# Kernel tuning notes

Hardware: AMD Instinct MI355X
Metric: run time of the kernel (lower is better)

The kernel has to match this reference:

```python
import jax, jax.numpy as jnp
import numpy as np

NEG_SLOPE = 0.2  # PyG GATConv leaky_relu slope
N_NODE = 1000   # nodes per graph (= n_nodes ctor arg = lstm1 input_size)
BATCH = 32      # num_graphs
C = 32          # in_channels == GAT out_channels per head
HEADS = 8
E = 384000      # total edges over the batched graph
H1, H2 = 32, 128
N_PRED = 2
N = N_NODE * BATCH


def _lstm(x_seq, W_ih, W_hh, b_ih, b_hh):
    # x_seq: [T, B, In]; PyTorch gate order i,f,g,o
    B = x_seq.shape[1]
    Hd = W_hh.shape[1]
    h0 = jnp.zeros((B, Hd), x_seq.dtype)

    def step(carry, x_t):
        h, c = carry
        g = x_t @ W_ih.T + h @ W_hh.T + b_ih + b_hh
        i, f, gg, o = jnp.split(g, 4, axis=-1)
        c = jax.nn.sigmoid(f) * c + jax.nn.sigmoid(i) * jnp.tanh(gg)
        h = jax.nn.sigmoid(o) * jnp.tanh(c)
        return (h, c), h

    (_, _), hs = jax.lax.scan(step, (h0, h0), x_seq)
    return hs


def setup_inputs() -> dict:
    key = jax.random.key(0)
    ks = jax.random.split(key, 20)
    inp = {}
    inp["x"] = jax.random.normal(ks[0], (N, C), jnp.float32)
    inp["src"] = jax.random.randint(ks[1], (E,), 0, N)
    inp["dst"] = jax.random.randint(ks[2], (E,), 0, N)
    inp["batch_size"] = BATCH
    # GATConv params (concat=False: mean over heads)
    inp["W_gat"] = jax.random.normal(ks[3], (C, HEADS * C), jnp.float32) * 0.1
    inp["a_src"] = jax.random.normal(ks[4], (HEADS, C), jnp.float32) * 0.1
    inp["a_dst"] = jax.random.normal(ks[5], (HEADS, C), jnp.float32) * 0.1
    inp["b_gat"] = jnp.zeros((C,), jnp.float32)
    # LSTM1: input N_NODE -> hidden 32
    inp["W_ih1"] = jax.random.normal(ks[6], (4 * H1, N_NODE), jnp.float32) * 0.05
    inp["W_hh1"] = jax.random.normal(ks[7], (4 * H1, H1), jnp.float32) * 0.1
    inp["b_ih1"] = jnp.zeros((4 * H1,), jnp.float32)
    inp["b_hh1"] = jnp.zeros((4 * H1,), jnp.float32)
    # LSTM2: input 32 -> hidden 128 (repaired from buggy source)
    inp["W_ih2"] = jax.random.normal(ks[8], (4 * H2, H1), jnp.float32) * 0.1
    inp["W_hh2"] = jax.random.normal(ks[9], (4 * H2, H2), jnp.float32) * 0.08
    inp["b_ih2"] = jnp.zeros((4 * H2,), jnp.float32)
    inp["b_hh2"] = jnp.zeros((4 * H2,), jnp.float32)
    # Linear head: 128 -> n_nodes * n_pred
    inp["W_lin"] = jax.random.normal(ks[10], (N_NODE * N_PRED, H2), jnp.float32) * 0.08
    inp["b_lin"] = jnp.zeros((N_NODE * N_PRED,), jnp.float32)
    return inp


def reference(x, src, dst, batch_size, W_gat, a_src, a_dst, b_gat,
              W_ih1, W_hh1, b_ih1, b_hh1, W_ih2, W_hh2, b_ih2, b_hh2,
              W_lin, b_lin):
    n, c = x.shape
    h = a_src.shape[0]
    # --- GATConv ---
    x_lin = (x @ W_gat).reshape(n, h, c)               # [N, H, C]
    asrc = jnp.einsum('nhc,hc->nh', x_lin, a_src)      # [N, H]
    adst = jnp.einsum('nhc,hc->nh', x_lin, a_dst)
    e = jax.nn.leaky_relu(asrc[src] + adst[dst], NEG_SLOPE)   # [E, H]
    m = jax.ops.segment_max(e, dst, num_segments=n)
    m = jnp.where(jnp.isfinite(m), m, 0.0)             # isolated nodes
    ew = jnp.exp(e - m[dst])
    denom = jax.ops.segment_sum(ew, dst, num_segments=n)
    alpha = ew / jnp.maximum(denom[dst], 1e-16)        # segment softmax
    agg = jax.ops.segment_sum(alpha[:, :, None] * x_lin[src], dst, num_segments=n)
    out = agg.mean(axis=1) + b_gat                     # concat=False -> head mean; [N, C]
    # --- reshape: seq over feature dim, LSTM input = nodes-per-graph ---
    n_node = n // batch_size
    seq = jnp.moveaxis(out.reshape(batch_size, n_node, c), 2, 0)  # [C, B, n_node]
    h1 = _lstm(seq, W_ih1, W_hh1, b_ih1, b_hh1)
    h2 = _lstm(h1, W_ih2, W_hh2, b_ih2, b_hh2)
    last = h2[-1]                                       # [B, 128]
    y = last @ W_lin.T + b_lin                          # [B, n_node*n_pred]
    return y.reshape(batch_size * n_node, -1)           # [B*n_node, n_pred]
```

## Files before the change

### kernel.cpp

```cpp
#include <hip/hip_runtime.h>
#include <hip/hip_fp16.h>
#include <math.h>

#define NEG_SLOPE 0.2f

__device__ __forceinline__ float sigm(float x) { return 1.0f / (1.0f + __expf(-x)); }
__device__ __forceinline__ float tanh_fast(float x) {
    float xc = fminf(fmaxf(x, -15.0f), 15.0f);
    float e2 = __expf(2.0f * xc);
    return (e2 - 1.0f) / (e2 + 1.0f);
}
__device__ __forceinline__ float lrelu(float x) { return (x > 0.0f) ? x : NEG_SLOPE * x; }

typedef _Float16 h2v __attribute__((ext_vector_type(2)));
__device__ __forceinline__ float fdot2h(h2v a, h2v b, float c) {
#if __has_builtin(__builtin_amdgcn_fdot2)
    return __builtin_amdgcn_fdot2(a, b, c, false);
#else
    return (float)a[0] * (float)b[0] + (float)a[1] * (float)b[1] + c;
#endif
}

__device__ __forceinline__ float dot16(const uint4& w, const uint4& h, float acc) {
    const h2v* wp = reinterpret_cast<const h2v*>(&w);
    const h2v* hp = reinterpret_cast<const h2v*>(&h);
    acc = fdot2h(wp[0], hp[0], acc);
    acc = fdot2h(wp[1], hp[1], acc);
    acc = fdot2h(wp[2], hp[2], acc);
    acc = fdot2h(wp[3], hp[3], acc);
    return acc;
}

__global__ void k_zero(int* __restrict__ deg, int N) {
    int i = blockIdx.x * 256 + threadIdx.x;
    if (i < N) deg[i] = 0;
}

__global__ void k_hist(const int* __restrict__ dst, int* __restrict__ deg, int E) {
    int e = blockIdx.x * 256 + threadIdx.x;
    if (e < E) atomicAdd(deg + dst[e], 1);
}

__global__ __launch_bounds__(256) void k_scan1(const int* __restrict__ deg,
                                               int* __restrict__ blksum, int N) {
    __shared__ int s[256];
    int tid = threadIdx.x;
    int i = blockIdx.x * 256 + tid;
    int v = (i < N) ? deg[i] : 0;
    s[tid] = v;
    __syncthreads();
    #pragma unroll
    for (int off = 128; off > 0; off >>= 1) {
        if (tid < off) s[tid] += s[tid + off];
        __syncthreads();
    }
    if (tid == 0) blksum[blockIdx.x] = s[0];
}

__global__ __launch_bounds__(256) void k_scan2(const int* __restrict__ blksum,
                                               int* __restrict__ blkoff, int nb) {
    __shared__ int s[256];
    int tid = threadIdx.x;
    int v = (tid < nb) ? blksum[tid] : 0;
    s[tid] = v;
    __syncthreads();
    for (int off = 1; off < 256; off <<= 1) {
        int t = (tid >= off) ? s[tid - off] : 0;
        __syncthreads();
        s[tid] += t;
        __syncthreads();
    }
    if (tid < nb) blkoff[tid] = s[tid] - v;
}

__global__ __launch_bounds__(256) void k_scan3(const int* __restrict__ deg,
                                               const int* __restrict__ blkoff,
                                               int* __restrict__ rowptr,
                                               int* __restrict__ cursor, int N, int E) {
    __shared__ int s[256];
    int tid = threadIdx.x;
    int i = blockIdx.x * 256 + tid;
    int v = (i < N) ? deg[i] : 0;
    s[tid] = v;
    __syncthreads();
    for (int off = 1; off < 256; off <<= 1) {
        int t = (tid >= off) ? s[tid - off] : 0;
        __syncthreads();
        s[tid] += t;
        __syncthreads();
    }
    int excl = s[tid] - v + blkoff[blockIdx.x];
    if (i < N) { rowptr[i] = excl; cursor[i] = excl; }
    if (i == N - 1) rowptr[N] = E;
}

__global__ void k_scatter(const int* __restrict__ src, const int* __restrict__ dst,
                          int* __restrict__ cursor, int* __restrict__ csr_src, int E) {
    int e = blockIdx.x * 256 + threadIdx.x;
    if (e < E) {
        int pos = atomicAdd(cursor + dst[e], 1);
        csr_src[pos] = src[e];
    }
}

__global__ void k_pre(const float* __restrict__ W_gat, const float* __restrict__ a_src,
                      const float* __restrict__ a_dst, float* __restrict__ wa) {
    int tid = threadIdx.x;
    int k = tid >> 3, h = tid & 7;
    float s1 = 0.0f, s2 = 0.0f;
    for (int c = 0; c < 32; ++c) {
        float wv = W_gat[k * 256 + h * 32 + c];
        s1 += wv * a_src[h * 32 + c];
        s2 += wv * a_dst[h * 32 + c];
    }
    wa[tid] = s1;
    wa[256 + tid] = s2;
}

__global__ __launch_bounds__(256) void k_att(const float* __restrict__ x,
                                             const float* __restrict__ wa,
                                             float* __restrict__ asrc,
                                             float* __restrict__ adst) {
    __shared__ float xs[32 * 33];
    __shared__ float was[256], wad[256];
    int tid = threadIdx.x;
    int n0 = blockIdx.x * 32;
    for (int i = tid; i < 1024; i += 256) {
        int nl = i >> 5, k = i & 31;
        xs[nl * 33 + k] = x[(size_t)(n0 + nl) * 32 + k];
    }
    was[tid] = wa[tid];
    wad[tid] = wa[256 + tid];
    __syncthreads();
    int nl = tid >> 3, h = tid & 7;
    float s1 = 0.0f, s2 = 0.0f;
    #pragma unroll
    for (int k = 0; k < 32; ++k) {
        float xv = xs[nl * 33 + k];
        s1 += xv * was[k * 8 + h];
        s2 += xv * wad[k * 8 + h];
    }
    asrc[(size_t)(n0 + nl) * 8 + h] = s1;
    adst[(size_t)(n0 + nl) * 8 + h] = s2;
}

__global__ __launch_bounds__(256) void k_gat(
    const int* __restrict__ rowptr, const int* __restrict__ csr_src,
    const float* __restrict__ asrc, const float* __restrict__ adst,
    const float* __restrict__ x, float* __restrict__ z, int N) {
    int w = (blockIdx.x * 256 + threadIdx.x) >> 6;
    int lane = threadIdx.x & 63;
    if (w >= N) return;
    int r0 = rowptr[w], r1 = rowptr[w + 1];
    int h = lane >> 3, kq = lane & 7;
    float ad = adst[w * 8 + h];
    float4 acc = make_float4(0.0f, 0.0f, 0.0f, 0.0f);
    float den = 0.0f;
    const float4* x4 = (const float4*)x;
    for (int i = r0; i < r1; i += 8) {
        int rem = r1 - i;
        int s0 = csr_src[i];
        int s1 = (rem > 1) ? csr_src[i + 1] : s0;
        int s2 = (rem > 2) ? csr_src[i + 2] : s0;
        int s3 = (rem > 3) ? csr_src[i + 3] : s0;
        int s4 = (rem > 4) ? csr_src[i + 4] : s0;
        int s5 = (rem > 5) ? csr_src[i + 5] : s0;
        int s6 = (rem > 6) ? csr_src[i + 6] : s0;
        int s7 = (rem > 7) ? csr_src[i + 7] : s0;
        float a0 = asrc[s0 * 8 + h], a1 = asrc[s1 * 8 + h];
        float a2 = asrc[s2 * 8 + h], a3 = asrc[s3 * 8 + h];
        float a4 = asrc[s4 * 8 + h], a5 = asrc[s5 * 8 + h];
        float a6 = asrc[s6 * 8 + h], a7 = asrc[s7 * 8 + h];
        float4 v0 = x4[(size_t)s0 * 8 + kq], v1 = x4[(size_t)s1 * 8 + kq];
        float4 v2 = x4[(size_t)s2 * 8 + kq], v3 = x4[(size_t)s3 * 8 + kq];
        float4 v4 = x4[(size_t)s4 * 8 + kq], v5 = x4[(size_t)s5 * 8 + kq];
        float4 v6 = x4[(size_t)s6 * 8 + kq], v7 = x4[(size_t)s7 * 8 + kq];
        float e0 = __expf(lrelu(a0 + ad));
        float e1 = (rem > 1) ? __expf(lrelu(a1 + ad)) : 0.0f;
        float e2 = (rem > 2) ? __expf(lrelu(a2 + ad)) : 0.0f;
        float e3 = (rem > 3) ? __expf(lrelu(a3 + ad)) : 0.0f;
        float e4 = (rem > 4) ? __expf(lrelu(a4 + ad)) : 0.0f;
        float e5 = (rem > 5) ? __expf(lrelu(a5 + ad)) : 0.0f;
        float e6 = (rem > 6) ? __expf(lrelu(a6 + ad)) : 0.0f;
        float e7 = (rem > 7) ? __expf(lrelu(a7 + ad)) : 0.0f;
        acc.x += e0 * v0.x + e1 * v1.x + e2 * v2.x + e3 * v3.x
               + e4 * v4.x + e5 * v5.x + e6 * v6.x + e7 * v7.x;
        acc.y += e0 * v0.y + e1 * v1.y + e2 * v2.y + e3 * v3.y
               + e4 * v4.y + e5 * v5.y + e6 * v6.y + e7 * v7.y;
        acc.z += e0 * v0.z + e1 * v1.z + e2 * v2.z + e3 * v3.z
               + e4 * v4.z + e5 * v5.z + e6 * v6.z + e7 * v7.z;
        acc.w += e0 * v0.w + e1 * v1.w + e2 * v2.w + e3 * v3.w
               + e4 * v4.w + e5 * v5.w + e6 * v6.w + e7 * v7.w;
        den += ((e0 + e1) + (e2 + e3)) + ((e4 + e5) + (e6 + e7));
    }
    float inv = 1.0f / fmaxf(den, 1e-16f);
    float4 r = make_float4(acc.x * inv, acc.y * inv, acc.z * inv, acc.w * inv);
    ((float4*)z)[(size_t)w * 64 + lane] = r;
}

__global__ __launch_bounds__(256) void k_zw(
    const float* __restrict__ z, const float* __restrict__ W_gat,
    const float* __restrict__ b_gat, float* __restrict__ gatT, int N, int n_node) {
    int gw = (blockIdx.x * 256 + threadIdx.x) >> 6;
    int lane = threadIdx.x & 63;
    int chalf = gw & 1;
    int nset = gw >> 1;
    int c = chalf * 16 + (lane & 15);
    int sl = lane >> 4;
    float wcol[64];
    #pragma unroll
    for (int i = 0; i < 64; ++i) {
        int k = i & 31, hh = sl * 2 + (i >> 5);
        wcol[i] = 0.125f * W_gat[k * 256 + hh * 32 + c];
    }
    float bg = b_gat[c];
    const float4* z4 = (const float4*)z;
    #pragma unroll 2
    for (int it = 0; it < 8; ++it) {
        int n = nset * 8 + it;
        float p = 0.0f;
        #pragma unroll
        for (int k4 = 0; k4 < 16; ++k4) {
            float4 zv = z4[(size_t)n * 64 + sl * 16 + k4];
            p += zv.x * wcol[4 * k4] + zv.y * wcol[4 * k4 + 1]
               + zv.z * wcol[4 * k4 + 2] + zv.w * wcol[4 * k4 + 3];
        }
        p += __shfl_xor(p, 16, 64);
        p += __shfl_xor(p, 32, 64);
        if (lane < 16) {
            int b = n / n_node, kk = n - b * n_node;
            gatT[((size_t)b * 32 + c) * n_node + kk] = p + bg;
        }
    }
}

__global__ __launch_bounds__(256) void k_wt(const float* __restrict__ W,
                                            float* __restrict__ Wt, int n_node) {
    __shared__ float tle[32][33];
    int kt = blockIdx.x & 31;
    int gt = blockIdx.x >> 5;
    int tid = threadIdx.x;
    for (int i = tid; i < 1024; i += 256) {
        int gl = i >> 5, kl = i & 31;
        int g = gt * 32 + gl, k = kt * 32 + kl;
        tle[gl][kl] = (k < n_node) ? W[(size_t)g * n_node + k] : 0.0f;
    }
    __syncthreads();
    for (int i = tid; i < 1024; i += 256) {
        int kl = i >> 5, gl = i & 31;
        int k = kt * 32 + kl, g = gt * 32 + gl;
        if (k < n_node) Wt[(size_t)k * 128 + g] = tle[gl][kl];
    }
}

__global__ __launch_bounds__(256) void k_pack2(
    const float* __restrict__ W_hh2, const float* __restrict__ W_ih2,
    const float* __restrict__ W_hh1,
    uint4* __restrict__ wc2p, uint4* __restrict__ wi2p, uint4* __restrict__ w1p) {
    int i = blockIdx.x * 256 + threadIdx.x;
    __align__(16) _Float16 tmp[8];
    if (i < 8192) {
        int jj = i >> 8, t = i & 255;
        int p = jj >> 4, j = jj & 15;
        int r = (t & 1) * 256 + p * 128 + (t >> 1);
        const float* s = W_hh2 + (size_t)r * 128 + j * 8;
        #pragma unroll
        for (int k = 0; k < 8; ++k) tmp[k] = (_Float16)s[k];
        wc2p[jj * 256 + t] = *(const uint4*)tmp;
    } else if (i < 10240) {
        int ii = i - 8192;
        int jj = ii >> 8, t = ii & 255;
        int p = jj >> 2, j = jj & 3;
        int r = (t & 1) * 256 + p * 128 + (t >> 1);
        const float* s = W_ih2 + (size_t)r * 32 + j * 8;
        #pragma unroll
        for (int k = 0; k < 8; ++k) tmp[k] = (_Float16)s[k];
        wi2p[jj * 256 + t] = *(const uint4*)tmp;
    } else if (i < 10752) {
        int ii = i - 10240;
        int jj = ii >> 6, l = ii & 63;
        int p = jj >> 2, j = jj & 3;
        int r = p * 64 + l;
        const float* s = W_hh1 + (size_t)r * 32 + j * 8;
        #pragma unroll
        for (int k = 0; k < 8; ++k) tmp[k] = (_Float16)s[k];
        w1p[jj * 64 + l] = *(const uint4*)tmp;
    }
}

__global__ __launch_bounds__(256) void k_p1(
    const float* __restrict__ gatT, const float* __restrict__ Wt,
    const float* __restrict__ b_ih1, const float* __restrict__ b_hh1,
    float* __restrict__ P1, int n_node, int B) {
    __shared__ __align__(16) float Arow[2][1024];
    __shared__ __align__(16) float part[4][2][128];
    int blk = blockIdx.x;
    int b = blk >> 4;
    int tq = blk & 15;
    int tid = threadIdx.x;
    const float* A0 = gatT + ((size_t)b * 32 + tq * 2) * n_node;
    #pragma unroll
    for (int r = 0; r < 2; ++r)
        for (int i = tid; i < n_node; i += 256)
            Arow[r][i] = A0[(size_t)r * n_node + i];
    __syncthreads();

    int g4 = tid & 31;
    int tloc = (tid >> 5) & 1;
    int ks = tid >> 6;
    int kq = n_node >> 2;
    int k0 = ks * kq;
    const float4* Wt4 = (const float4*)Wt;
    float4 acc = make_float4(0.0f, 0.0f, 0.0f, 0.0f);
    #pragma unroll 4
    for (int k = 0; k < kq; ++k) {
        float4 w = Wt4[(size_t)(k0 + k) * 32 + g4];
        float a = Arow[tloc][k0 + k];
        acc.x += w.x * a; acc.y += w.y * a;
        acc.z += w.z * a; acc.w += w.w * a;
    }
    *(float4*)&part[ks][tloc][g4 * 4] = acc;
    __syncthreads();

    int tl = tid >> 7, g = tid & 127;
    float s = part[0][tl][g] + part[1][tl][g] + part[2][tl][g] + part[3][tl][g]
            + b_ih1[g] + b_hh1[g];
    int t = tq * 2 + tl;
    P1[((size_t)t * B + b) * 128 + g] = s;
}

__global__ __launch_bounds__(256, 1) void k_lstm(
    const float* __restrict__ P1, const uint4* __restrict__ wc2p,
    const uint4* __restrict__ wi2p, const uint4* __restrict__ w1p,
    const float* __restrict__ b_ih2, const float* __restrict__ b_hh2,
    float* __restrict__ h2finT, int B, int T) {
    __shared__ __align__(16) float P1s[32][128];
    __shared__ __align__(16) __half h1buf[2][32];
    __shared__ __align__(16) __half h2buf[2][128];
    int t = threadIdx.x, b = blockIdx.x;
    int u = t >> 1, ht = t & 1;

    for (int i = t; i < 1024; i += 256) {
        int tt = i >> 5, c4 = i & 31;
        ((float4*)P1s[tt])[c4] = ((const float4*)(P1 + ((size_t)tt * B + b) * 128))[c4];
    }
    uint4 wc[32];
    #pragma unroll
    for (int j = 0; j < 32; ++j) wc[j] = wc2p[j * 256 + t];
    uint4 wi[8];
    #pragma unroll
    for (int j = 0; j < 8; ++j) wi[j] = wi2p[j * 256 + t];
    uint4 w1[8];
    if (t < 64) {
        #pragma unroll
        for (int j = 0; j < 8; ++j) w1[j] = w1p[j * 64 + t];
    }
    int r0 = ht * 256 + u;
    int r1 = ht * 256 + 128 + u;
    float bias0 = b_ih2[r0] + b_hh2[r0];
    float bias1 = b_ih2[r1] + b_hh2[r1];

    if (t < 32) h1buf[0][t] = __float2half(0.0f);
    if (t < 128) h2buf[0][t] = __float2half(0.0f);
    float c1 = 0.0f, c2 = 0.0f;
    __syncthreads();

    for (int s = 0; s <= T; ++s) {
        const uint4* h1q = (const uint4*)h1buf[s & 1];
        uint4 hv0 = h1q[0], hv1 = h1q[1], hv2 = h1q[2], hv3 = h1q[3];

        if (s >= 1) {
            int t2 = s - 1;
            const uint4* hb = (const uint4*)h2buf[t2 & 1];
            float p0a, p0b, p1a, p1b;
            p0a = dot16(wi[0], hv0, 0.0f); p0b = dot16(wi[1], hv1, 0.0f);
            p0a = dot16(wi[2], hv2, p0a);  p0b = dot16(wi[3], hv3, p0b);
            p1a = dot16(wi[4], hv0, 0.0f); p1b = dot16(wi[5], hv1, 0.0f);
            p1a = dot16(wi[6], hv2, p1a);  p1b = dot16(wi[7], hv3, p1b);
            #pragma unroll
            for (int c = 0; c < 4; ++c) {
                uint4 h0 = hb[c * 4], h1_ = hb[c * 4 + 1];
                uint4 h2_ = hb[c * 4 + 2], h3 = hb[c * 4 + 3];
                p0a = dot16(wc[c * 4], h0, p0a);
                p0b = dot16(wc[c * 4 + 1], h1_, p0b);
                p0a = dot16(wc[c * 4 + 2], h2_, p0a);
                p0b = dot16(wc[c * 4 + 3], h3, p0b);
                p1a = dot16(wc[16 + c * 4], h0, p1a);
                p1b = dot16(wc[16 + c * 4 + 1], h1_, p1b);
                p1a = dot16(wc[16 + c * 4 + 2], h2_, p1a);
                p1b = dot16(wc[16 + c * 4 + 3], h3, p1b);
            }
            float s0 = p0a + p0b + bias0;
            float s1 = p1a + p1b + bias1;
            float o0 = __shfl_xor(s0, 1, 64);
            float o1 = __shfl_xor(s1, 1, 64);
            float gi = (ht == 0) ? s0 : o0;
            float gf = (ht == 0) ? s1 : o1;
            float gg = (ht == 0) ? o0 : s0;
            float go = (ht == 0) ? o1 : s1;
            c2 = sigm(gf) * c2 + sigm(gi) * tanh_fast(gg);
            float h = sigm(go) * tanh_fast(c2);
            if (ht == 0) {
                h2buf[(t2 + 1) & 1][u] = __float2half(h);
                if (t2 == T - 1) h2finT[u * 32 + b] = h;
            }
        }
        if (t < 64 && s < T) {
            float aA = P1s[s][t];
            float aB = P1s[s][64 + t];
            aA = dot16(w1[0], hv0, aA); aA = dot16(w1[1], hv1, aA);
            aA = dot16(w1[2], hv2, aA); aA = dot16(w1[3], hv3, aA);
            aB = dot16(w1[4], hv0, aB); aB = dot16(w1[5], hv1, aB);
            aB = dot16(w1[6], hv2, aB); aB = dot16(w1[7], hv3, aB);
            float oA = __shfl_xor(aA, 32, 64);
            float oB = __shfl_xor(aB, 32, 64);
            float gi = (t < 32) ? aA : oA;
            float gf = (t < 32) ? oA : aA;
            float gg = (t < 32) ? aB : oB;
            float go = (t < 32) ? oB : aB;
            c1 = sigm(gf) * c1 + sigm(gi) * tanh_fast(gg);
            float h = sigm(go) * tanh_fast(c1);
            if (t < 32) h1buf[(s + 1) & 1][t] = __float2half(h);
        }
        __syncthreads();
    }
}

__global__ __launch_bounds__(256) void k_fin(
    const float* __restrict__ h2finT, const float* __restrict__ W_lin,
    const float* __restrict__ b_lin, float* __restrict__ out, int n_node, int B) {
    __shared__ __align__(16) float hs[128];
    int b = blockIdx.x >> 3;
    int kc = blockIdx.x & 7;
    int tid = threadIdx.x;
    if (tid < 128) hs[tid] = h2finT[tid * 32 + b];
    __syncthreads();
    int outdim = n_node * 2;
    int kk = kc * 256 + tid;
    if (kk < outdim) {
        float acc = b_lin[kk];
        const float4* W4 = (const float4*)(W_lin + (size_t)kk * 128);
        const float4* h4 = (const float4*)hs;
        #pragma unroll 8
        for (int j = 0; j < 32; ++j) {
            float4 w = W4[j], h = h4[j];
            acc += w.x * h.x + w.y * h.y + w.z * h.z + w.w * h.w;
        }
        out[(size_t)b * outdim + kk] = acc;
    }
}

extern "C" void kernel_launch(void* const* d_in, const int* in_sizes, int n_in,
                              void* d_out, int out_size, void* d_ws, size_t ws_size,
                              hipStream_t stream) {
    const float* x     = (const float*)d_in[0];
    const int*   src   = (const int*)d_in[1];
    const int*   dst   = (const int*)d_in[2];
    const float* W_gat = (const float*)d_in[4];
    const float* a_src = (const float*)d_in[5];
    const float* a_dst = (const float*)d_in[6];
    const float* b_gat = (const float*)d_in[7];
    const float* W_ih1 = (const float*)d_in[8];
    const float* W_hh1 = (const float*)d_in[9];
    const float* b_ih1 = (const float*)d_in[10];
    const float* b_hh1 = (const float*)d_in[11];
    const float* W_ih2 = (const float*)d_in[12];
    const float* W_hh2 = (const float*)d_in[13];
    const float* b_ih2 = (const float*)d_in[14];
    const float* b_hh2 = (const float*)d_in[15];
    const float* W_lin = (const float*)d_in[16];
    const float* b_lin = (const float*)d_in[17];

    int N = in_sizes[0] / 32;
    int E = in_sizes[1];
    int n_node = in_sizes[8] / 128;
    int B = N / n_node;
    int T = 32;

    float* ws = (float*)d_ws;
    float* z      = ws;
    float* asrc   = z + (size_t)N * 256;
    float* adst   = asrc + (size_t)N * 8;
    float* gatT   = adst + (size_t)N * 8;
    float* P1     = gatT + (size_t)N * 32;
    float* wc2f   = P1 + (size_t)T * B * 128;
    float* wiff   = wc2f + 32768;
    float* w1ff   = wiff + 8192;
    float* h2finT = w1ff + 2048;
    float* wa     = h2finT + 128 * 32;
    int* deg     = (int*)(wa + 512);
    int* cursor  = deg + N;
    int* rowptr  = cursor + N;
    int* csr_src = rowptr + N + 1;
    int* blksum  = csr_src + E;
    int* blkoff  = blksum + 256;
    float* Wt    = (float*)(((uintptr_t)(blkoff + 256) + 255) & ~(uintptr_t)255);

    uint4* wc2p = (uint4*)wc2f;
    uint4* wi2p = (uint4*)wiff;
    uint4* w1p  = (uint4*)w1ff;

    int nb = (N + 255) / 256;

    k_pack2<<<42, 256, 0, stream>>>(W_hh2, W_ih2, W_hh1, wc2p, wi2p, w1p);
    k_wt<<<128, 256, 0, stream>>>(W_ih1, Wt, n_node);
    k_zero<<<(N + 255) / 256, 256, 0, stream>>>(deg, N);
    k_hist<<<(E + 255) / 256, 256, 0, stream>>>(dst, deg, E);
    k_scan1<<<nb, 256, 0, stream>>>(deg, blksum, N);
    k_scan2<<<1, 256, 0, stream>>>(blksum, blkoff, nb);
    k_scan3<<<nb, 256, 0, stream>>>(deg, blkoff, rowptr, cursor, N, E);
    k_scatter<<<(E + 255) / 256, 256, 0, stream>>>(src, dst, cursor, csr_src, E);
    k_pre<<<1, 256, 0, stream>>>(W_gat, a_src, a_dst, wa);
    k_att<<<N / 32, 256, 0, stream>>>(x, wa, asrc, adst);
    k_gat<<<(N * 64 + 255) / 256, 256, 0, stream>>>(rowptr, csr_src, asrc, adst,
                                                    x, z, N);
    k_zw<<<2000, 256, 0, stream>>>(z, W_gat, b_gat, gatT, N, n_node);
    k_p1<<<B * 16, 256, 0, stream>>>(gatT, Wt, b_ih1, b_hh1, P1, n_node, B);
    k_lstm<<<B, 256, 0, stream>>>(P1, wc2p, wi2p, w1p, b_ih2, b_hh2, h2finT, B, T);
    k_fin<<<B * 8, 256, 0, stream>>>(h2finT, W_lin, b_lin, (float*)d_out, n_node, B);
}
```

Baseline: 207.5 us.

## Merge prep kernels into one launch and move half of LSTM2 weights to LDS

Four small preprocessing kernels (weight transpose, fp16 weight packing, attention-weight precompute, degree zeroing) are folded into a single launch dispatched by block index, which removes several launch gaps from the serial stream. Separately, the LSTM kernel keeps only half of the recurrent W_hh2 fragments in registers and stages the other half in 64KB of shared memory. This lowers register pressure but adds LDS reads to every recurrent step, and the larger LDS footprint may limit occupancy (one block per graph anyway).

```diff
diff --git a/kernel.cpp b/kernel.cpp
--- a/kernel.cpp
+++ b/kernel.cpp
@@ -29,11 +29,6 @@
     acc = fdot2h(wp[2], hp[2], acc);
     acc = fdot2h(wp[3], hp[3], acc);
     return acc;
-}
-
-__global__ void k_zero(int* __restrict__ deg, int N) {
-    int i = blockIdx.x * 256 + threadIdx.x;
-    if (i < N) deg[i] = 0;
 }
 
 __global__ void k_hist(const int* __restrict__ dst, int* __restrict__ deg, int E) {
@@ -103,18 +98,74 @@
     }
 }
 
-__global__ void k_pre(const float* __restrict__ W_gat, const float* __restrict__ a_src,
-                      const float* __restrict__ a_dst, float* __restrict__ wa) {
-    int tid = threadIdx.x;
-    int k = tid >> 3, h = tid & 7;
-    float s1 = 0.0f, s2 = 0.0f;
-    for (int c = 0; c < 32; ++c) {
-        float wv = W_gat[k * 256 + h * 32 + c];
-        s1 += wv * a_src[h * 32 + c];
-        s2 += wv * a_dst[h * 32 + c];
-    }
-    wa[tid] = s1;
-    wa[256 + tid] = s2;
+__global__ __launch_bounds__(256) void k_prep(
+    const float* __restrict__ W_ih1, float* __restrict__ Wt, int n_node,
+    const float* __restrict__ W_hh2, const float* __restrict__ W_ih2,
+    const float* __restrict__ W_hh1,
+    uint4* __restrict__ wc2p, uint4* __restrict__ wi2p, uint4* __restrict__ w1p,
+    const float* __restrict__ W_gat, const float* __restrict__ a_src,
+    const float* __restrict__ a_dst, float* __restrict__ wa,
+    int* __restrict__ deg, int N) {
+    int blk = blockIdx.x, tid = threadIdx.x;
+    if (blk < 128) {
+        __shared__ float tle[32][33];
+        int kt = blk & 31;
+        int gt = blk >> 5;
+        for (int i = tid; i < 1024; i += 256) {
+            int gl = i >> 5, kl = i & 31;
+            int g = gt * 32 + gl, k = kt * 32 + kl;
+            tle[gl][kl] = (k < n_node) ? W_ih1[(size_t)g * n_node + k] : 0.0f;
+        }
+        __syncthreads();
+        for (int i = tid; i < 1024; i += 256) {
+            int kl = i >> 5, gl = i & 31;
+            int k = kt * 32 + kl, g = gt * 32 + gl;
+            if (k < n_node) Wt[(size_t)k * 128 + g] = tle[gl][kl];
+        }
+    } else if (blk < 170) {
+        int i = (blk - 128) * 256 + tid;
+        __align__(16) _Float16 tmp[8];
+        if (i < 8192) {
+            int jj = i >> 8, t = i & 255;
+            int p = jj >> 4, j = jj & 15;
+            int r = (t & 1) * 256 + p * 128 + (t >> 1);
+            const float* s = W_hh2 + (size_t)r * 128 + j * 8;
+            #pragma unroll
+            for (int k = 0; k < 8; ++k) tmp[k] = (_Float16)s[k];
+            wc2p[jj * 256 + t] = *(const uint4*)tmp;
+        } else if (i < 10240) {
+            int ii = i - 8192;
+            int jj = ii >> 8, t = ii & 255;
+            int p = jj >> 2, j = jj & 3;
+            int r = (t & 1) * 256 + p * 128 + (t >> 1);
+            const float* s = W_ih2 + (size_t)r * 32 + j * 8;
+            #pragma unroll
+            for (int k = 0; k < 8; ++k) tmp[k] = (_Float16)s[k];
+            wi2p[jj * 256 + t] = *(const uint4*)tmp;
+        } else if (i < 10752) {
+            int ii = i - 10240;
+            int jj = ii >> 6, l = ii & 63;
+            int p = jj >> 2, j = jj & 3;
+            int r = p * 64 + l;
+            const float* s = W_hh1 + (size_t)r * 32 + j * 8;
+            #pragma unroll
+            for (int k = 0; k < 8; ++k) tmp[k] = (_Float16)s[k];
+            w1p[jj * 64 + l] = *(const uint4*)tmp;
+        }
+    } else if (blk == 170) {
+        int k = tid >> 3, h = tid & 7;
+        float s1 = 0.0f, s2 = 0.0f;
+        for (int c = 0; c < 32; ++c) {
+            float wv = W_gat[k * 256 + h * 32 + c];
+            s1 += wv * a_src[h * 32 + c];
+            s2 += wv * a_dst[h * 32 + c];
+        }
+        wa[tid] = s1;
+        wa[256 + tid] = s2;
+    } else {
+        int i = (blk - 171) * 256 + tid;
+        if (i < N) deg[i] = 0;
+    }
 }
 
 __global__ __launch_bounds__(256) void k_att(const float* __restrict__ x,
@@ -234,60 +285,6 @@
     }
 }
 
-__global__ __launch_bounds__(256) void k_wt(const float* __restrict__ W,
-                                            float* __restrict__ Wt, int n_node) {
-    __shared__ float tle[32][33];
-    int kt = blockIdx.x & 31;
-    int gt = blockIdx.x >> 5;
-    int tid = threadIdx.x;
-    for (int i = tid; i < 1024; i += 256) {
-        int gl = i >> 5, kl = i & 31;
-        int g = gt * 32 + gl, k = kt * 32 + kl;
-        tle[gl][kl] = (k < n_node) ? W[(size_t)g * n_node + k] : 0.0f;
-    }
-    __syncthreads();
-    for (int i = tid; i < 1024; i += 256) {
-        int kl = i >> 5, gl = i & 31;
-        int k = kt * 32 + kl, g = gt * 32 + gl;
-        if (k < n_node) Wt[(size_t)k * 128 + g] = tle[gl][kl];
-    }
-}
-
-__global__ __launch_bounds__(256) void k_pack2(
-    const float* __restrict__ W_hh2, const float* __restrict__ W_ih2,
-    const float* __restrict__ W_hh1,
-    uint4* __restrict__ wc2p, uint4* __restrict__ wi2p, uint4* __restrict__ w1p) {
-    int i = blockIdx.x * 256 + threadIdx.x;
-    __align__(16) _Float16 tmp[8];
-    if (i < 8192) {
-        int jj = i >> 8, t = i & 255;
-        int p = jj >> 4, j = jj & 15;
-        int r = (t & 1) * 256 + p * 128 + (t >> 1);
-        const float* s = W_hh2 + (size_t)r * 128 + j * 8;
-        #pragma unroll
-        for (int k = 0; k < 8; ++k) tmp[k] = (_Float16)s[k];
-        wc2p[jj * 256 + t] = *(const uint4*)tmp;
-    } else if (i < 10240) {
-        int ii = i - 8192;
-        int jj = ii >> 8, t = ii & 255;
-        int p = jj >> 2, j = jj & 3;
-        int r = (t & 1) * 256 + p * 128 + (t >> 1);
-        const float* s = W_ih2 + (size_t)r * 32 + j * 8;
-        #pragma unroll
-        for (int k = 0; k < 8; ++k) tmp[k] = (_Float16)s[k];
-        wi2p[jj * 256 + t] = *(const uint4*)tmp;
-    } else if (i < 10752) {
-        int ii = i - 10240;
-        int jj = ii >> 6, l = ii & 63;
-        int p = jj >> 2, j = jj & 3;
-        int r = p * 64 + l;
-        const float* s = W_hh1 + (size_t)r * 32 + j * 8;
-        #pragma unroll
-        for (int k = 0; k < 8; ++k) tmp[k] = (_Float16)s[k];
-        w1p[jj * 64 + l] = *(const uint4*)tmp;
-    }
-}
-
 __global__ __launch_bounds__(256) void k_p1(
     const float* __restrict__ gatT, const float* __restrict__ Wt,
     const float* __restrict__ b_ih1, const float* __restrict__ b_hh1,
@@ -334,6 +331,7 @@
     const uint4* __restrict__ wi2p, const uint4* __restrict__ w1p,
     const float* __restrict__ b_ih2, const float* __restrict__ b_hh2,
     float* __restrict__ h2finT, int B, int T) {
+    __shared__ uint4 wlds[16 * 256];
     __shared__ __align__(16) float P1s[32][128];
     __shared__ __align__(16) __half h1buf[2][32];
     __shared__ __align__(16) __half h2buf[2][128];
@@ -344,9 +342,11 @@
         int tt = i >> 5, c4 = i & 31;
         ((float4*)P1s[tt])[c4] = ((const float4*)(P1 + ((size_t)tt * B + b) * 128))[c4];
     }
-    uint4 wc[32];
-    #pragma unroll
-    for (int j = 0; j < 32; ++j) wc[j] = wc2p[j * 256 + t];
+    uint4 wc[16];
+    #pragma unroll
+    for (int j = 0; j < 16; ++j) wc[j] = wc2p[j * 256 + t];
+    #pragma unroll
+    for (int j = 0; j < 16; ++j) wlds[j * 256 + t] = wc2p[(16 + j) * 256 + t];
     uint4 wi[8];
     #pragma unroll
     for (int j = 0; j < 8; ++j) wi[j] = wi2p[j * 256 + t];
@@ -381,14 +381,18 @@
             for (int c = 0; c < 4; ++c) {
                 uint4 h0 = hb[c * 4], h1_ = hb[c * 4 + 1];
                 uint4 h2_ = hb[c * 4 + 2], h3 = hb[c * 4 + 3];
+                uint4 wB0 = wlds[(c * 4 + 0) * 256 + t];
+                uint4 wB1 = wlds[(c * 4 + 1) * 256 + t];
+                uint4 wB2 = wlds[(c * 4 + 2) * 256 + t];
+                uint4 wB3 = wlds[(c * 4 + 3) * 256 + t];
                 p0a = dot16(wc[c * 4], h0, p0a);
                 p0b = dot16(wc[c * 4 + 1], h1_, p0b);
                 p0a = dot16(wc[c * 4 + 2], h2_, p0a);
                 p0b = dot16(wc[c * 4 + 3], h3, p0b);
-                p1a = dot16(wc[16 + c * 4], h0, p1a);
-                p1b = dot16(wc[16 + c * 4 + 1], h1_, p1b);
-                p1a = dot16(wc[16 + c * 4 + 2], h2_, p1a);
-                p1b = dot16(wc[16 + c * 4 + 3], h3, p1b);
+                p1a = dot16(wB0, h0, p1a);
+                p1b = dot16(wB1, h1_, p1b);
+                p1a = dot16(wB2, h2_, p1a);
+                p1b = dot16(wB3, h3, p1b);
             }
             float s0 = p0a + p0b + bias0;
             float s1 = p1a + p1b + bias1;
@@ -502,15 +506,14 @@
 
     int nb = (N + 255) / 256;
 
-    k_pack2<<<42, 256, 0, stream>>>(W_hh2, W_ih2, W_hh1, wc2p, wi2p, w1p);
-    k_wt<<<128, 256, 0, stream>>>(W_ih1, Wt, n_node);
-    k_zero<<<(N + 255) / 256, 256, 0, stream>>>(deg, N);
+    k_prep<<<171 + nb, 256, 0, stream>>>(W_ih1, Wt, n_node, W_hh2, W_ih2, W_hh1,
+                                         wc2p, wi2p, w1p, W_gat, a_src, a_dst,
+                                         wa, deg, N);
     k_hist<<<(E + 255) / 256, 256, 0, stream>>>(dst, deg, E);
     k_scan1<<<nb, 256, 0, stream>>>(deg, blksum, N);
     k_scan2<<<1, 256, 0, stream>>>(blksum, blkoff, nb);
     k_scan3<<<nb, 256, 0, stream>>>(deg, blkoff, rowptr, cursor, N, E);
     k_scatter<<<(E + 255) / 256, 256, 0, stream>>>(src, dst, cursor, csr_src, E);
-    k_pre<<<1, 256, 0, stream>>>(W_gat, a_src, a_dst, wa);
     k_att<<<N / 32, 256, 0, stream>>>(x, wa, asrc, adst);
     k_gat<<<(N * 64 + 255) / 256, 256, 0, stream>>>(rowptr, csr_src, asrc, adst,
                                                     x, z, N);
```

Result: faster. 202.2 us (-2.5%).
